# Performance work log

Measured on AMD Instinct MI355X. Metric: run time of the kernel, lower is better.

Reference implementation:

```python
import jax, jax.numpy as jnp
import numpy as np

N_NODES = 100000
N_EDGES = 3200000
N_FEAT = 512
HIDDEN = 16
N_CLASSES = 8


def setup_inputs() -> dict:
    key = jax.random.key(0)
    ks = jax.random.split(key, 7)
    x = jax.random.normal(ks[0], (N_NODES, N_FEAT), dtype=jnp.float32)
    edge_index = jax.random.randint(ks[1], (2, N_EDGES), 0, N_NODES, dtype=jnp.int64)
    # original code scales weights by /100; uniform weights are equivalent for testing
    edges_weight = jax.random.uniform(ks[2], (N_EDGES,), dtype=jnp.float32)
    # Glorot-ish params for the two GCNConv layers
    W1 = jax.random.normal(ks[3], (N_FEAT, HIDDEN), dtype=jnp.float32) / np.sqrt(N_FEAT)
    b1 = jnp.zeros((HIDDEN,), dtype=jnp.float32)
    W2 = jax.random.normal(ks[4], (HIDDEN, N_CLASSES), dtype=jnp.float32) / np.sqrt(HIDDEN)
    b2 = jnp.zeros((N_CLASSES,), dtype=jnp.float32)
    return {"x": x, "edge_index": edge_index, "edges_weight": edges_weight,
            "W1": W1, "b1": b1, "W2": W2, "b2": b2}


def _gcn_norm(edge_index, edges_weight, num_nodes):
    """PyG GCNConv normalization: add self-loops (weight 1), then
    norm_e = d^{-1/2}[src] * w_e * d^{-1/2}[dst] with d = weighted degree."""
    loop = jnp.arange(num_nodes, dtype=edge_index.dtype)
    src = jnp.concatenate([edge_index[0], loop])
    dst = jnp.concatenate([edge_index[1], loop])
    w = jnp.concatenate([edges_weight, jnp.ones((num_nodes,), edges_weight.dtype)])
    deg = jax.ops.segment_sum(w, dst, num_segments=num_nodes)
    dis = jnp.where(deg > 0, jax.lax.rsqrt(deg), 0.0)  # deg_inv_sqrt
    norm = dis[src] * w * dis[dst]
    return src, dst, norm


def _gcn_layer(h, W, b, src, dst, norm, num_nodes):
    h = h @ W                                 # transform first (small msg dim)
    msg = h[src] * norm[:, None]              # gather + edge scaling
    out = jax.ops.segment_sum(msg, dst, num_segments=num_nodes)  # scatter-add
    return out + b


def reference(x, edge_index, edges_weight, W1, b1, W2, b2):
    n = x.shape[0]
    src, dst, norm = _gcn_norm(edge_index, edges_weight, n)
    h = _gcn_layer(x, W1, b1, src, dst, norm, n)
    h = jax.nn.relu(h)
    h = _gcn_layer(h, W2, b2, src, dst, norm, n)
    return jax.nn.log_softmax(h, axis=1)
```

## Files before the change

kernel.cpp:

```cpp
#include <hip/hip_runtime.h>

#define TPB 256
constexpr int HID = 16;
constexpr int NC  = 8;

__device__ __forceinline__ void atomAddF(float* p, float v) {
    unsafeAtomicAdd(p, v);
}

__global__ void detect64_kernel(const int* __restrict__ ei, int E, int* flag) {
    int l = threadIdx.x;
    int v = 0;
    if (l < 32 && 2 * l + 1 < 2 * E) v = ei[2 * l + 1];
    unsigned long long b = __ballot(v != 0);
    if (l == 0) *flag = (b == 0ULL) ? 1 : 0;
}

__device__ __forceinline__ int edge_at(const int* __restrict__ ei, int index, int is64) {
    return is64 ? ei[2 * index] : ei[index];
}


__global__ void init_deg_kernel(float* deg, int N) {
    int i = blockIdx.x * TPB + threadIdx.x;
    if (i < N) deg[i] = 1.0f;
}

__global__ void init_nd_kernel(float* deg, int* cnt, int N) {
    int i = blockIdx.x * TPB + threadIdx.x;
    if (i < N) { deg[i] = 1.0f; cnt[i] = 0; }
}

__global__ void init_cnt_kernel(int* cnt, int N) {
    int i = blockIdx.x * TPB + threadIdx.x;
    if (i < N) cnt[i] = 0;
}

__global__ void dis_kernel(float* deg, int N) {
    int i = blockIdx.x * TPB + threadIdx.x;
    if (i < N) deg[i] = rsqrtf(deg[i]);
}

__global__ void gemm1_kernel(const float* __restrict__ x, const float* __restrict__ W,
                             float* __restrict__ h, int N, int K) {
    int row = blockIdx.x * TPB + threadIdx.x;
    if (row >= N) return;
    const float* xr = x + (size_t)row * K;
    float acc[HID];
#pragma unroll
    for (int j = 0; j < HID; ++j) acc[j] = 0.f;
    for (int k = 0; k < K; k += 4) {
        float4 xv = *reinterpret_cast<const float4*>(xr + k);
        const float* Wk = W + (size_t)k * HID;
#pragma unroll
        for (int kk = 0; kk < 4; ++kk) {
            float xs = (&xv.x)[kk];
#pragma unroll
            for (int j = 0; j < HID; ++j)
                acc[j] = fmaf(xs, Wk[kk * HID + j], acc[j]);
        }
    }
    float* hr = h + (size_t)row * HID;
#pragma unroll
    for (int j = 0; j < HID; j += 4)
        *reinterpret_cast<float4*>(hr + j) = make_float4(acc[j], acc[j+1], acc[j+2], acc[j+3]);
}

__global__ void gemm1s_kernel(const float* __restrict__ x, const float* __restrict__ W,
                              const float* __restrict__ dis, float* __restrict__ h, int N, int K) {
    int row = blockIdx.x * TPB + threadIdx.x;
    if (row >= N) return;
    const float* xr = x + (size_t)row * K;
    float acc[HID];
#pragma unroll
    for (int j = 0; j < HID; ++j) acc[j] = 0.f;
    for (int k = 0; k < K; k += 4) {
        float4 xv = *reinterpret_cast<const float4*>(xr + k);
        const float* Wk = W + (size_t)k * HID;
#pragma unroll
        for (int kk = 0; kk < 4; ++kk) {
            float xs = (&xv.x)[kk];
#pragma unroll
            for (int j = 0; j < HID; ++j)
                acc[j] = fmaf(xs, Wk[kk * HID + j], acc[j]);
        }
    }
    float d = dis[row];
#pragma unroll
    for (int j = 0; j < HID; ++j) acc[j] *= d;
    float* hr = h + (size_t)row * HID;
#pragma unroll
    for (int j = 0; j < HID; j += 4)
        *reinterpret_cast<float4*>(hr + j) = make_float4(acc[j], acc[j+1], acc[j+2], acc[j+3]);
}

__global__ void gemm2_kernel(const float* __restrict__ agg1, const float* __restrict__ W2,
                             float* __restrict__ h2, int N) {
    int i = blockIdx.x * TPB + threadIdx.x;
    if (i >= N) return;
    const float* a = agg1 + (size_t)i * HID;
    float hv[HID];
#pragma unroll
    for (int k = 0; k < HID; k += 4) {
        float4 v = *reinterpret_cast<const float4*>(a + k);
        hv[k]     = fmaxf(v.x, 0.f);
        hv[k + 1] = fmaxf(v.y, 0.f);
        hv[k + 2] = fmaxf(v.z, 0.f);
        hv[k + 3] = fmaxf(v.w, 0.f);
    }
    float acc[NC];
#pragma unroll
    for (int c = 0; c < NC; ++c) acc[c] = 0.f;
#pragma unroll
    for (int k = 0; k < HID; ++k)
#pragma unroll
        for (int c = 0; c < NC; ++c)
            acc[c] = fmaf(hv[k], W2[k * NC + c], acc[c]);
    float* o = h2 + (size_t)i * NC;
    *reinterpret_cast<float4*>(o)     = make_float4(acc[0], acc[1], acc[2], acc[3]);
    *reinterpret_cast<float4*>(o + 4) = make_float4(acc[4], acc[5], acc[6], acc[7]);
}

__global__ void gemm2s_kernel(const float* __restrict__ agg1, const float* __restrict__ W2,
                              const float* __restrict__ dis, float* __restrict__ h2, int N) {
    int i = blockIdx.x * TPB + threadIdx.x;
    if (i >= N) return;
    const float* a = agg1 + (size_t)i * HID;
    float hv[HID];
#pragma unroll
    for (int k = 0; k < HID; k += 4) {
        float4 v = *reinterpret_cast<const float4*>(a + k);
        hv[k]     = fmaxf(v.x, 0.f);
        hv[k + 1] = fmaxf(v.y, 0.f);
        hv[k + 2] = fmaxf(v.z, 0.f);
        hv[k + 3] = fmaxf(v.w, 0.f);
    }
    float acc[NC];
#pragma unroll
    for (int c = 0; c < NC; ++c) acc[c] = 0.f;
#pragma unroll
    for (int k = 0; k < HID; ++k)
#pragma unroll
        for (int c = 0; c < NC; ++c)
            acc[c] = fmaf(hv[k], W2[k * NC + c], acc[c]);
    float d = dis[i];
#pragma unroll
    for (int c = 0; c < NC; ++c) acc[c] *= d;
    float* o = h2 + (size_t)i * NC;
    *reinterpret_cast<float4*>(o)     = make_float4(acc[0], acc[1], acc[2], acc[3]);
    *reinterpret_cast<float4*>(o + 4) = make_float4(acc[4], acc[5], acc[6], acc[7]);
}


__global__ void scatterP_kernel(const int* __restrict__ ei, const float* __restrict__ w,
                                int* __restrict__ cnt, uint2* __restrict__ edata,
                                int E, int C, const int* __restrict__ flag) {
    int e = blockIdx.x * TPB + threadIdx.x;
    if (e >= E) return;
    int is64 = *flag;
    int src = edge_at(ei, e, is64);
    int dst = edge_at(ei, E + e, is64);
    float wv = w[e];
    int pos = atomicAdd(&cnt[dst], 1);
    if (pos < C)
        edata[(size_t)dst * C + pos] = make_uint2((unsigned)src, __float_as_uint(wv));
}

__global__ void degP_kernel(const uint2* __restrict__ edata, const int* __restrict__ cnt,
                            float* __restrict__ dis, int N, int C) {
    int wid = (blockIdx.x * blockDim.x + threadIdx.x) >> 6;
    if (wid >= N) return;
    int lane = threadIdx.x & 63;
    int m = cnt[wid]; if (m > C) m = C;
    const uint2* seg = edata + (size_t)wid * C;
    float s = 0.f;
    for (int i = lane; i < m; i += 64) s += __uint_as_float(seg[i].y);
#pragma unroll
    for (int o = 1; o < 64; o <<= 1) s += __shfl_xor(s, o, 64);
    if (lane == 0) dis[wid] = rsqrtf(1.0f + s);
}

__global__ void agg1P_kernel(const uint2* __restrict__ edata, const int* __restrict__ cnt,
                             const float* __restrict__ h1s, const float* __restrict__ dis,
                             const float* __restrict__ b1, float* __restrict__ agg1,
                             int N, int C) {
    int wid = (blockIdx.x * blockDim.x + threadIdx.x) >> 6;
    if (wid >= N) return;
    int lane = threadIdx.x & 63;
    int m = cnt[wid]; if (m > C) m = C;
    const uint2* seg = edata + (size_t)wid * C;
    float acc[HID];
#pragma unroll
    for (int j = 0; j < HID; ++j) acc[j] = 0.f;
    for (int i = lane; i < m; i += 64) {
        uint2 u = seg[i];
        float wv = __uint_as_float(u.y);
        const float* hr = h1s + (size_t)u.x * HID;
        float4 a = *reinterpret_cast<const float4*>(hr);
        float4 b = *reinterpret_cast<const float4*>(hr + 4);
        float4 c = *reinterpret_cast<const float4*>(hr + 8);
        float4 d = *reinterpret_cast<const float4*>(hr + 12);
        acc[0]  = fmaf(wv, a.x, acc[0]);  acc[1]  = fmaf(wv, a.y, acc[1]);
        acc[2]  = fmaf(wv, a.z, acc[2]);  acc[3]  = fmaf(wv, a.w, acc[3]);
        acc[4]  = fmaf(wv, b.x, acc[4]);  acc[5]  = fmaf(wv, b.y, acc[5]);
        acc[6]  = fmaf(wv, b.z, acc[6]);  acc[7]  = fmaf(wv, b.w, acc[7]);
        acc[8]  = fmaf(wv, c.x, acc[8]);  acc[9]  = fmaf(wv, c.y, acc[9]);
        acc[10] = fmaf(wv, c.z, acc[10]); acc[11] = fmaf(wv, c.w, acc[11]);
        acc[12] = fmaf(wv, d.x, acc[12]); acc[13] = fmaf(wv, d.y, acc[13]);
        acc[14] = fmaf(wv, d.z, acc[14]); acc[15] = fmaf(wv, d.w, acc[15]);
    }
#pragma unroll
    for (int j = 0; j < HID; ++j) {
        acc[j] += __shfl_xor(acc[j], 16, 64);
        acc[j] += __shfl_xor(acc[j], 32, 64);
    }
#pragma unroll
    for (int t = 0; t < 8; ++t) {
        float lo = __shfl_xor(acc[t], 8, 64);
        float hi = __shfl_xor(acc[t + 8], 8, 64);
        acc[t] = (lane & 8) ? (acc[t + 8] + hi) : (acc[t] + lo);
    }
#pragma unroll
    for (int t = 0; t < 4; ++t) {
        float lo = __shfl_xor(acc[t], 4, 64);
        float hi = __shfl_xor(acc[t + 4], 4, 64);
        acc[t] = (lane & 4) ? (acc[t + 4] + hi) : (acc[t] + lo);
    }
#pragma unroll
    for (int t = 0; t < 2; ++t) {
        float lo = __shfl_xor(acc[t], 2, 64);
        float hi = __shfl_xor(acc[t + 2], 2, 64);
        acc[t] = (lane & 2) ? (acc[t + 2] + hi) : (acc[t] + lo);
    }
    {
        float lo = __shfl_xor(acc[0], 1, 64);
        float hi = __shfl_xor(acc[1], 1, 64);
        acc[0] = (lane & 1) ? (acc[1] + hi) : (acc[0] + lo);
    }
    if (lane < HID) {
        float dd = dis[wid];
        agg1[(size_t)wid * HID + lane] =
            b1[lane] + dd * (h1s[(size_t)wid * HID + lane] + acc[0]);
    }
}

__global__ void agg2P_lsm_kernel(const uint2* __restrict__ edata, const int* __restrict__ cnt,
                                 const float* __restrict__ h2s, const float* __restrict__ dis,
                                 const float* __restrict__ b2, float* __restrict__ out,
                                 int N, int C) {
    int wid = (blockIdx.x * blockDim.x + threadIdx.x) >> 6;
    if (wid >= N) return;
    int lane = threadIdx.x & 63;
    int m = cnt[wid]; if (m > C) m = C;
    const uint2* seg = edata + (size_t)wid * C;
    float acc[NC];
#pragma unroll
    for (int j = 0; j < NC; ++j) acc[j] = 0.f;
    for (int i = lane; i < m; i += 64) {
        uint2 u = seg[i];
        float wv = __uint_as_float(u.y);
        const float* hr = h2s + (size_t)u.x * NC;
        float4 a = *reinterpret_cast<const float4*>(hr);
        float4 b = *reinterpret_cast<const float4*>(hr + 4);
        acc[0] = fmaf(wv, a.x, acc[0]);  acc[1] = fmaf(wv, a.y, acc[1]);
        acc[2] = fmaf(wv, a.z, acc[2]);  acc[3] = fmaf(wv, a.w, acc[3]);
        acc[4] = fmaf(wv, b.x, acc[4]);  acc[5] = fmaf(wv, b.y, acc[5]);
        acc[6] = fmaf(wv, b.z, acc[6]);  acc[7] = fmaf(wv, b.w, acc[7]);
    }
#pragma unroll
    for (int j = 0; j < NC; ++j) {
        acc[j] += __shfl_xor(acc[j], 8, 64);
        acc[j] += __shfl_xor(acc[j], 16, 64);
        acc[j] += __shfl_xor(acc[j], 32, 64);
    }
#pragma unroll
    for (int t = 0; t < 4; ++t) {
        float lo = __shfl_xor(acc[t], 4, 64);
        float hi = __shfl_xor(acc[t + 4], 4, 64);
        acc[t] = (lane & 4) ? (acc[t + 4] + hi) : (acc[t] + lo);
    }
#pragma unroll
    for (int t = 0; t < 2; ++t) {
        float lo = __shfl_xor(acc[t], 2, 64);
        float hi = __shfl_xor(acc[t + 2], 2, 64);
        acc[t] = (lane & 2) ? (acc[t + 2] + hi) : (acc[t] + lo);
    }
    {
        float lo = __shfl_xor(acc[0], 1, 64);
        float hi = __shfl_xor(acc[1], 1, 64);
        acc[0] = (lane & 1) ? (acc[1] + hi) : (acc[0] + lo);
    }
    int c = lane & 7;
    float dd = dis[wid];
    float v = b2[c] + dd * (h2s[(size_t)wid * NC + c] + acc[0]);
    float mx = v;
    mx = fmaxf(mx, __shfl_xor(mx, 1, 64));
    mx = fmaxf(mx, __shfl_xor(mx, 2, 64));
    mx = fmaxf(mx, __shfl_xor(mx, 4, 64));
    float ex = expf(v - mx);
    float ssum = ex;
    ssum += __shfl_xor(ssum, 1, 64);
    ssum += __shfl_xor(ssum, 2, 64);
    ssum += __shfl_xor(ssum, 4, 64);
    float r = v - mx - logf(ssum);
    if (lane < NC) out[(size_t)wid * NC + lane] = r;
}


__global__ void hist_deg_kernel(const int* __restrict__ ei, const float* __restrict__ w,
                                int* __restrict__ cnt, float* __restrict__ deg,
                                int E, const int* __restrict__ flag) {
    int e = blockIdx.x * TPB + threadIdx.x;
    if (e >= E) return;
    int is64 = *flag;
    int dst = edge_at(ei, E + e, is64);
    atomicAdd(&cnt[dst], 1);
    atomAddF(&deg[dst], w[e]);
}

__global__ void scanA_kernel(const int* __restrict__ cnt, int* __restrict__ bsum, int N) {
    int i = blockIdx.x * 256 + threadIdx.x;
    int v = (i < N) ? cnt[i] : 0;
#pragma unroll
    for (int o = 32; o > 0; o >>= 1) v += __shfl_down(v, o, 64);
    __shared__ int ws[4];
    if ((threadIdx.x & 63) == 0) ws[threadIdx.x >> 6] = v;
    __syncthreads();
    if (threadIdx.x == 0) bsum[blockIdx.x] = ws[0] + ws[1] + ws[2] + ws[3];
}

__global__ void scanB_kernel(int* __restrict__ bsum, int NB, int* __restrict__ rowoffN, int E) {
    __shared__ int s[1024];
    int t = threadIdx.x;
    int v = (t < NB) ? bsum[t] : 0;
    s[t] = v;
    __syncthreads();
    for (int o = 1; o < 1024; o <<= 1) {
        int u = (t >= o) ? s[t - o] : 0;
        __syncthreads();
        s[t] += u;
        __syncthreads();
    }
    if (t < NB) bsum[t] = s[t] - v;
    if (t == 0) *rowoffN = E;
}

__global__ void scanC_kernel(const int* __restrict__ cnt, const int* __restrict__ bsum,
                             int* __restrict__ rowoff, int* __restrict__ cursor, int N) {
    __shared__ int s[256];
    int b = blockIdx.x, t = threadIdx.x;
    int i = b * 256 + t;
    int v = (i < N) ? cnt[i] : 0;
    s[t] = v;
    __syncthreads();
    for (int o = 1; o < 256; o <<= 1) {
        int u = (t >= o) ? s[t - o] : 0;
        __syncthreads();
        s[t] += u;
        __syncthreads();
    }
    if (i < N) {
        int ex = bsum[b] + s[t] - v;
        rowoff[i] = ex;
        cursor[i] = ex;
    }
}

__global__ void scatter_kernel(const int* __restrict__ ei, const float* __restrict__ w,
                               const float* __restrict__ dis, int* __restrict__ cursor,
                               int2* __restrict__ edata, int E, const int* __restrict__ flag) {
    int e = blockIdx.x * TPB + threadIdx.x;
    if (e >= E) return;
    int is64 = *flag;
    int src = edge_at(ei, e, is64);
    int dst = edge_at(ei, E + e, is64);
    float nrm = dis[src] * w[e] * dis[dst];
    int pos = atomicAdd(&cursor[dst], 1);
    edata[pos] = make_int2(src, __float_as_int(nrm));
}

__global__ void agg1_csr_kernel(const int2* __restrict__ edata, const int* __restrict__ rowoff,
                                const float* __restrict__ h1, const float* __restrict__ dis,
                                const float* __restrict__ b1, float* __restrict__ agg1, int N) {
    int wid = (blockIdx.x * blockDim.x + threadIdx.x) >> 6;
    if (wid >= N) return;
    int lane = threadIdx.x & 63;
    int j = lane & 15, g = lane >> 4;
    int s = rowoff[wid];
    int epd = rowoff[wid + 1] - s;
    float acc = 0.f;
    for (int i = g; i < epd; i += 4) {
        int2 d = edata[s + i];
        acc += __int_as_float(d.y) * h1[(size_t)d.x * HID + j];
    }
    acc += __shfl_xor(acc, 16, 64);
    acc += __shfl_xor(acc, 32, 64);
    if (g == 0) {
        float di = dis[wid];
        agg1[(size_t)wid * HID + j] = b1[j] + di * di * h1[(size_t)wid * HID + j] + acc;
    }
}

__global__ void agg2_lsm_kernel(const int2* __restrict__ edata, const int* __restrict__ rowoff,
                                const float* __restrict__ h2, const float* __restrict__ dis,
                                const float* __restrict__ b2, float* __restrict__ out, int N) {
    int wid = (blockIdx.x * blockDim.x + threadIdx.x) >> 6;
    if (wid >= N) return;
    int lane = threadIdx.x & 63;
    int j = lane & 7, g = lane >> 3;
    int s = rowoff[wid];
    int epd = rowoff[wid + 1] - s;
    float acc = 0.f;
    for (int i = g; i < epd; i += 8) {
        int2 d = edata[s + i];
        acc += __int_as_float(d.y) * h2[(size_t)d.x * NC + j];
    }
    acc += __shfl_xor(acc, 8, 64);
    acc += __shfl_xor(acc, 16, 64);
    acc += __shfl_xor(acc, 32, 64);
    float di = dis[wid];
    float v = b2[j] + di * di * h2[(size_t)wid * NC + j] + acc;
    float mx = v;
    mx = fmaxf(mx, __shfl_xor(mx, 1, 64));
    mx = fmaxf(mx, __shfl_xor(mx, 2, 64));
    mx = fmaxf(mx, __shfl_xor(mx, 4, 64));
    float ex = expf(v - mx);
    float ssum = ex;
    ssum += __shfl_xor(ssum, 1, 64);
    ssum += __shfl_xor(ssum, 2, 64);
    ssum += __shfl_xor(ssum, 4, 64);
    float r = v - mx - logf(ssum);
    if (g == 0) out[(size_t)wid * NC + j] = r;
}


__global__ void deg_edge_kernel(const int* __restrict__ ei, const float* __restrict__ w,
                                float* deg, int E, const int* __restrict__ flag) {
    int e = blockIdx.x * TPB + threadIdx.x;
    if (e >= E) return;
    int is64 = *flag;
    int dst = edge_at(ei, E + e, is64);
    atomAddF(&deg[dst], w[e]);
}

__global__ void init_agg1_kernel(const float* __restrict__ h1, const float* __restrict__ dis,
                                 const float* __restrict__ b1, float* __restrict__ agg1, int N) {
    int t = blockIdx.x * TPB + threadIdx.x;
    if (t >= N * HID) return;
    int i = t >> 4, j = t & 15;
    float d = dis[i];
    agg1[t] = b1[j] + d * d * h1[t];
}

__global__ void edge1_kernel(const int* __restrict__ ei, const float* __restrict__ w,
                             const float* __restrict__ dis, const float* __restrict__ h1,
                             float* __restrict__ agg1, int E, const int* __restrict__ flag) {
    int t = blockIdx.x * TPB + threadIdx.x;
    if (t >= E * HID) return;
    int e = t >> 4, j = t & 15;
    int is64 = *flag;
    int src = edge_at(ei, e, is64);
    int dst = edge_at(ei, E + e, is64);
    float nrm = dis[src] * w[e] * dis[dst];
    atomAddF(&agg1[dst * HID + j], nrm * h1[src * HID + j]);
}

__global__ void init_out_kernel(const float* __restrict__ h2, const float* __restrict__ dis,
                                const float* __restrict__ b2, float* __restrict__ out, int N) {
    int t = blockIdx.x * TPB + threadIdx.x;
    if (t >= N * NC) return;
    int i = t >> 3, j = t & 7;
    float d = dis[i];
    out[t] = b2[j] + d * d * h2[t];
}

__global__ void edge2_kernel(const int* __restrict__ ei, const float* __restrict__ w,
                             const float* __restrict__ dis, const float* __restrict__ h2,
                             float* __restrict__ out, int E, const int* __restrict__ flag) {
    int t = blockIdx.x * TPB + threadIdx.x;
    if (t >= E * NC) return;
    int e = t >> 3, j = t & 7;
    int is64 = *flag;
    int src = edge_at(ei, e, is64);
    int dst = edge_at(ei, E + e, is64);
    float nrm = dis[src] * w[e] * dis[dst];
    atomAddF(&out[dst * NC + j], nrm * h2[src * NC + j]);
}

__global__ void lsm_kernel(float* __restrict__ out, int N) {
    int i = blockIdx.x * TPB + threadIdx.x;
    if (i >= N) return;
    float* r = out + (size_t)i * NC;
    float4 a = *reinterpret_cast<const float4*>(r);
    float4 b = *reinterpret_cast<const float4*>(r + 4);
    float v[NC] = {a.x, a.y, a.z, a.w, b.x, b.y, b.z, b.w};
    float m = v[0];
#pragma unroll
    for (int j = 1; j < NC; ++j) m = fmaxf(m, v[j]);
    float s = 0.f;
#pragma unroll
    for (int j = 0; j < NC; ++j) s += expf(v[j] - m);
    float lse = m + logf(s);
#pragma unroll
    for (int j = 0; j < NC; ++j) v[j] -= lse;
    *reinterpret_cast<float4*>(r)     = make_float4(v[0], v[1], v[2], v[3]);
    *reinterpret_cast<float4*>(r + 4) = make_float4(v[4], v[5], v[6], v[7]);
}

extern "C" void kernel_launch(void* const* d_in, const int* in_sizes, int n_in,
                              void* d_out, int out_size, void* d_ws, size_t ws_size,
                              hipStream_t stream) {
    const float* x  = (const float*)d_in[0];
    const int*   ei = (const int*)d_in[1];
    const float* w  = (const float*)d_in[2];
    const float* W1 = (const float*)d_in[3];
    const float* b1 = (const float*)d_in[4];
    const float* W2 = (const float*)d_in[5];
    const float* b2 = (const float*)d_in[6];
    float* out = (float*)d_out;

    int E = in_sizes[2];
    int N = out_size / NC;
    int K = in_sizes[0] / N;

    auto nb = [](long long n) { return (int)((n + TPB - 1) / TPB); };
    int waveblocks = (int)(((long long)N * 64 + TPB - 1) / TPB);

    int C = 0;
    {
        int cands[3] = {96, 88, 80};
        for (int ci = 0; ci < 3; ++ci) {
            size_t need = (size_t)4 * ((size_t)2 * N * cands[ci] + (size_t)42 * N + 1);
            if (ws_size >= need) { C = cands[ci]; break; }
        }
    }

    if (C > 0) {
        uint2* edata = (uint2*)d_ws;
        float* h1s   = (float*)(edata + (size_t)N * C);
        float* agg1  = h1s + (size_t)N * HID;
        float* h2s   = agg1 + (size_t)N * HID;
        float* dis   = h2s + (size_t)N * NC;
        int*   cnt   = (int*)(dis + N);
        int*   flag  = cnt + N;

        detect64_kernel<<<1, 64, 0, stream>>>(ei, E, flag);
        init_cnt_kernel<<<nb(N), TPB, 0, stream>>>(cnt, N);
        scatterP_kernel<<<nb(E), TPB, 0, stream>>>(ei, w, cnt, edata, E, C, flag);
        degP_kernel<<<waveblocks, TPB, 0, stream>>>(edata, cnt, dis, N, C);
        gemm1s_kernel<<<nb(N), TPB, 0, stream>>>(x, W1, dis, h1s, N, K);
        agg1P_kernel<<<waveblocks, TPB, 0, stream>>>(edata, cnt, h1s, dis, b1, agg1, N, C);
        gemm2s_kernel<<<nb(N), TPB, 0, stream>>>(agg1, W2, dis, h2s, N);
        agg2P_lsm_kernel<<<waveblocks, TPB, 0, stream>>>(edata, cnt, h2s, dis, b2, out, N, C);
        return;
    }

    int NB = (N + 255) / 256;
    size_t need_csr = (size_t)4 * ((size_t)2 * E + (size_t)43 * N + 1026);
    bool use_csr = (ws_size >= need_csr) && (NB <= 1024);

    if (use_csr) {
        int2*  edata  = (int2*)d_ws;
        float* deg    = (float*)(edata + E);
        float* h1     = deg + N;
        float* agg1   = h1 + (size_t)N * HID;
        float* h2     = agg1 + (size_t)N * HID;
        int*   cnt    = (int*)(h2 + (size_t)N * NC);
        int*   rowoff = cnt + N;
        int*   cursor = rowoff + N + 1;
        int*   bsum   = cursor + N;
        int*   flag   = bsum + 1024;

        detect64_kernel<<<1, 64, 0, stream>>>(ei, E, flag);
        init_nd_kernel<<<nb(N), TPB, 0, stream>>>(deg, cnt, N);
        hist_deg_kernel<<<nb(E), TPB, 0, stream>>>(ei, w, cnt, deg, E, flag);
        dis_kernel<<<nb(N), TPB, 0, stream>>>(deg, N);
        scanA_kernel<<<NB, 256, 0, stream>>>(cnt, bsum, N);
        scanB_kernel<<<1, 1024, 0, stream>>>(bsum, NB, rowoff + N, E);
        scanC_kernel<<<NB, 256, 0, stream>>>(cnt, bsum, rowoff, cursor, N);
        gemm1_kernel<<<nb(N), TPB, 0, stream>>>(x, W1, h1, N, K);
        scatter_kernel<<<nb(E), TPB, 0, stream>>>(ei, w, deg, cursor, edata, E, flag);
        agg1_csr_kernel<<<waveblocks, TPB, 0, stream>>>(edata, rowoff, h1, deg, b1, agg1, N);
        gemm2_kernel<<<nb(N), TPB, 0, stream>>>(agg1, W2, h2, N);
        agg2_lsm_kernel<<<waveblocks, TPB, 0, stream>>>(edata, rowoff, h2, deg, b2, out, N);
    } else {
        float* deg  = (float*)d_ws;
        float* h1   = deg + N;
        float* agg1 = h1 + (size_t)N * HID;
        float* h2   = agg1 + (size_t)N * HID;
        int*   flag = (int*)(h2 + (size_t)N * NC);

        detect64_kernel<<<1, 64, 0, stream>>>(ei, E, flag);
        init_deg_kernel<<<nb(N), TPB, 0, stream>>>(deg, N);
        deg_edge_kernel<<<nb(E), TPB, 0, stream>>>(ei, w, deg, E, flag);
        dis_kernel<<<nb(N), TPB, 0, stream>>>(deg, N);
        gemm1_kernel<<<nb(N), TPB, 0, stream>>>(x, W1, h1, N, K);
        init_agg1_kernel<<<nb((long long)N * HID), TPB, 0, stream>>>(h1, deg, b1, agg1, N);
        edge1_kernel<<<nb((long long)E * HID), TPB, 0, stream>>>(ei, w, deg, h1, agg1, E, flag);
        gemm2_kernel<<<nb(N), TPB, 0, stream>>>(agg1, W2, h2, N);
        init_out_kernel<<<nb((long long)N * NC), TPB, 0, stream>>>(h2, deg, b2, out, N);
        edge2_kernel<<<nb((long long)E * NC), TPB, 0, stream>>>(ei, w, deg, h2, out, E, flag);
        lsm_kernel<<<nb(N), TPB, 0, stream>>>(out, N);
    }
}
```

Measured before the change: 722.4 us.

## Compute first-layer GEMM with one wavefront per row and W in LDS

```diff
diff --git a/kernel.cpp b/kernel.cpp
--- a/kernel.cpp
+++ b/kernel.cpp
@@ -3,6 +3,7 @@
 #define TPB 256
 constexpr int HID = 16;
 constexpr int NC  = 8;
+constexpr int WPAD = 20;
 
 __device__ __forceinline__ void atomAddF(float* p, float v) {
     unsafeAtomicAdd(p, v);
@@ -92,6 +93,72 @@
 #pragma unroll
     for (int j = 0; j < HID; j += 4)
         *reinterpret_cast<float4*>(hr + j) = make_float4(acc[j], acc[j+1], acc[j+2], acc[j+3]);
+}
+
+__global__ void gemm1w_kernel(const float* __restrict__ x, const float* __restrict__ W,
+                              const float* __restrict__ dis, float* __restrict__ h,
+                              int N, int K, int nwaves) {
+    extern __shared__ float Wlds[];
+    int t = threadIdx.x;
+    for (int i = t; i < K * HID; i += TPB) {
+        int k = i >> 4, j = i & 15;
+        Wlds[k * WPAD + j] = W[i];
+    }
+    __syncthreads();
+    int lane = t & 63;
+    int gwave = (int)((blockIdx.x * (unsigned)TPB + t) >> 6);
+    for (int row = gwave; row < N; row += nwaves) {
+        const float* xr = x + (size_t)row * K;
+        float acc[HID];
+#pragma unroll
+        for (int j = 0; j < HID; ++j) acc[j] = 0.f;
+        for (int k0 = lane; k0 < K; k0 += 64) {
+            float xs = xr[k0];
+            const float* Wr = Wlds + k0 * WPAD;
+            float4 a = *reinterpret_cast<const float4*>(Wr);
+            float4 b = *reinterpret_cast<const float4*>(Wr + 4);
+            float4 c = *reinterpret_cast<const float4*>(Wr + 8);
+            float4 d = *reinterpret_cast<const float4*>(Wr + 12);
+            acc[0]  = fmaf(xs, a.x, acc[0]);  acc[1]  = fmaf(xs, a.y, acc[1]);
+            acc[2]  = fmaf(xs, a.z, acc[2]);  acc[3]  = fmaf(xs, a.w, acc[3]);
+            acc[4]  = fmaf(xs, b.x, acc[4]);  acc[5]  = fmaf(xs, b.y, acc[5]);
+            acc[6]  = fmaf(xs, b.z, acc[6]);  acc[7]  = fmaf(xs, b.w, acc[7]);
+            acc[8]  = fmaf(xs, c.x, acc[8]);  acc[9]  = fmaf(xs, c.y, acc[9]);
+            acc[10] = fmaf(xs, c.z, acc[10]); acc[11] = fmaf(xs, c.w, acc[11]);
+            acc[12] = fmaf(xs, d.x, acc[12]); acc[13] = fmaf(xs, d.y, acc[13]);
+            acc[14] = fmaf(xs, d.z, acc[14]); acc[15] = fmaf(xs, d.w, acc[15]);
+        }
+#pragma unroll
+        for (int j = 0; j < HID; ++j) {
+            acc[j] += __shfl_xor(acc[j], 16, 64);
+            acc[j] += __shfl_xor(acc[j], 32, 64);
+        }
+#pragma unroll
+        for (int tt = 0; tt < 8; ++tt) {
+            float lo = __shfl_xor(acc[tt], 8, 64);
+            float hi = __shfl_xor(acc[tt + 8], 8, 64);
+            acc[tt] = (lane & 8) ? (acc[tt + 8] + hi) : (acc[tt] + lo);
+        }
+#pragma unroll
+        for (int tt = 0; tt < 4; ++tt) {
+            float lo = __shfl_xor(acc[tt], 4, 64);
+            float hi = __shfl_xor(acc[tt + 4], 4, 64);
+            acc[tt] = (lane & 4) ? (acc[tt + 4] + hi) : (acc[tt] + lo);
+        }
+#pragma unroll
+        for (int tt = 0; tt < 2; ++tt) {
+            float lo = __shfl_xor(acc[tt], 2, 64);
+            float hi = __shfl_xor(acc[tt + 2], 2, 64);
+            acc[tt] = (lane & 2) ? (acc[tt + 2] + hi) : (acc[tt] + lo);
+        }
+        {
+            float lo = __shfl_xor(acc[0], 1, 64);
+            float hi = __shfl_xor(acc[1], 1, 64);
+            acc[0] = (lane & 1) ? (acc[1] + hi) : (acc[0] + lo);
+        }
+        if (lane < HID)
+            h[(size_t)row * HID + lane] = dis[row] * acc[0];
+    }
 }
 
 __global__ void gemm2_kernel(const float* __restrict__ agg1, const float* __restrict__ W2,
@@ -548,7 +615,16 @@
         init_cnt_kernel<<<nb(N), TPB, 0, stream>>>(cnt, N);
         scatterP_kernel<<<nb(E), TPB, 0, stream>>>(ei, w, cnt, edata, E, C, flag);
         degP_kernel<<<waveblocks, TPB, 0, stream>>>(edata, cnt, dis, N, C);
-        gemm1s_kernel<<<nb(N), TPB, 0, stream>>>(x, W1, dis, h1s, N, K);
+
+        size_t wlds_bytes = (size_t)K * WPAD * 4;
+        if ((K % 64) == 0 && wlds_bytes <= 64 * 1024) {
+            int g1blocks = 2048;
+            int nwaves = g1blocks * (TPB / 64);
+            gemm1w_kernel<<<g1blocks, TPB, wlds_bytes, stream>>>(x, W1, dis, h1s, N, K, nwaves);
+        } else {
+            gemm1s_kernel<<<nb(N), TPB, 0, stream>>>(x, W1, dis, h1s, N, K);
+        }
+
         agg1P_kernel<<<waveblocks, TPB, 0, stream>>>(edata, cnt, h1s, dis, b1, agg1, N, C);
         gemm2s_kernel<<<nb(N), TPB, 0, stream>>>(agg1, W2, dis, h2s, N);
         agg2P_lsm_kernel<<<waveblocks, TPB, 0, stream>>>(edata, cnt, h2s, dis, b2, out, N, C);
```

Measured after the change: 776.1 us. 1.07x slower.

## Replace per-node padded edge lists with block-partitioned edges and shared-memory aggregation

Applied to the files above, without the earlier changes.

```diff
diff --git a/kernel.cpp b/kernel.cpp
--- a/kernel.cpp
+++ b/kernel.cpp
@@ -3,6 +3,10 @@
 #define TPB 256
 constexpr int HID = 16;
 constexpr int NC  = 8;
+constexpr int NPB = 512;
+constexpr int LOG_NPB = 9;
+constexpr int MAXBK = 1024;
+constexpr int P1B = 512;
 
 __device__ __forceinline__ void atomAddF(float* p, float v) {
     unsafeAtomicAdd(p, v);
@@ -26,11 +30,6 @@
     if (i < N) deg[i] = 1.0f;
 }
 
-__global__ void init_nd_kernel(float* deg, int* cnt, int N) {
-    int i = blockIdx.x * TPB + threadIdx.x;
-    if (i < N) { deg[i] = 1.0f; cnt[i] = 0; }
-}
-
 __global__ void init_cnt_kernel(int* cnt, int N) {
     int i = blockIdx.x * TPB + threadIdx.x;
     if (i < N) cnt[i] = 0;
@@ -40,6 +39,7 @@
     int i = blockIdx.x * TPB + threadIdx.x;
     if (i < N) deg[i] = rsqrtf(deg[i]);
 }
+
 
 __global__ void gemm1_kernel(const float* __restrict__ x, const float* __restrict__ W,
                              float* __restrict__ h, int N, int K) {
@@ -149,6 +149,168 @@
     float* o = h2 + (size_t)i * NC;
     *reinterpret_cast<float4*>(o)     = make_float4(acc[0], acc[1], acc[2], acc[3]);
     *reinterpret_cast<float4*>(o + 4) = make_float4(acc[4], acc[5], acc[6], acc[7]);
+}
+
+
+__global__ void zero_tot_kernel(int* tot, int NBK) {
+    int i = blockIdx.x * TPB + threadIdx.x;
+    if (i < NBK) tot[i] = 0;
+}
+
+__global__ void p1hist_kernel(const int* __restrict__ ei, int* __restrict__ hist,
+                              int* __restrict__ tot, int E, int NBK,
+                              const int* __restrict__ flag) {
+    __shared__ int lh[MAXBK];
+    int t = threadIdx.x;
+    for (int i = t; i < NBK; i += TPB) lh[i] = 0;
+    __syncthreads();
+    int is64 = *flag;
+    int CH = (E + gridDim.x - 1) / gridDim.x;
+    int s = blockIdx.x * CH;
+    int e2 = min(E, s + CH);
+    for (int i = s + t; i < e2; i += TPB) {
+        int dst = edge_at(ei, E + i, is64);
+        atomicAdd(&lh[dst >> LOG_NPB], 1);
+    }
+    __syncthreads();
+    for (int i = t; i < NBK; i += TPB) {
+        int v = lh[i];
+        hist[(size_t)blockIdx.x * NBK + i] = v;
+        if (v) atomicAdd(&tot[i], v);
+    }
+}
+
+__global__ void p1scan_kernel(const int* __restrict__ tot, int* __restrict__ base,
+                              int* __restrict__ cursor, int NBK, int E) {
+    __shared__ int s[1024];
+    int t = threadIdx.x;
+    int v = (t < NBK) ? tot[t] : 0;
+    s[t] = v;
+    __syncthreads();
+    for (int o = 1; o < 1024; o <<= 1) {
+        int u = (t >= o) ? s[t - o] : 0;
+        __syncthreads();
+        s[t] += u;
+        __syncthreads();
+    }
+    if (t < NBK) { base[t] = s[t] - v; cursor[t] = s[t] - v; }
+    if (t == 0) base[NBK] = E;
+}
+
+__global__ void p1scatter_kernel(const int* __restrict__ ei, const float* __restrict__ w,
+                                 const int* __restrict__ hist, int* __restrict__ cursor,
+                                 uint2* __restrict__ part, int E, int NBK,
+                                 const int* __restrict__ flag) {
+    __shared__ int startk[MAXBK];
+    __shared__ int loc[MAXBK];
+    int t = threadIdx.x;
+    for (int i = t; i < NBK; i += TPB) {
+        int hv = hist[(size_t)blockIdx.x * NBK + i];
+        startk[i] = hv ? atomicAdd(&cursor[i], hv) : 0;
+        loc[i] = 0;
+    }
+    __syncthreads();
+    int is64 = *flag;
+    int CH = (E + gridDim.x - 1) / gridDim.x;
+    int s = blockIdx.x * CH;
+    int e2 = min(E, s + CH);
+    for (int i = s + t; i < e2; i += TPB) {
+        int src = edge_at(ei, i, is64);
+        int dst = edge_at(ei, E + i, is64);
+        float wv = w[i];
+        int k = dst >> LOG_NPB;
+        int dl = dst & (NPB - 1);
+        int pos = startk[k] + atomicAdd(&loc[k], 1);
+        part[pos] = make_uint2(__float_as_uint(wv), (unsigned)src | ((unsigned)dl << 17));
+    }
+}
+
+__global__ void degB_kernel(const uint2* __restrict__ part, const int* __restrict__ base,
+                            float* __restrict__ dis, int N) {
+    __shared__ float dacc[NPB];
+    int k = blockIdx.x, t = threadIdx.x;
+    for (int r = t; r < NPB; r += TPB) dacc[r] = 1.0f;
+    __syncthreads();
+    int s = base[k], e2 = base[k + 1];
+    for (int i = s + t; i < e2; i += TPB) {
+        uint2 en = part[i];
+        atomicAdd(&dacc[(en.y >> 17) & (NPB - 1)], __uint_as_float(en.x));
+    }
+    __syncthreads();
+    for (int r = t; r < NPB; r += TPB) {
+        int node = (k << LOG_NPB) + r;
+        if (node < N) dis[node] = rsqrtf(dacc[r]);
+    }
+}
+
+__global__ void aggB1_kernel(const uint2* __restrict__ part, const int* __restrict__ base,
+                             const float* __restrict__ h1s, const float* __restrict__ dis,
+                             const float* __restrict__ b1, float* __restrict__ agg1, int N) {
+    __shared__ float acc[NPB * 17];
+    int k = blockIdx.x, t = threadIdx.x;
+    for (int idx = t; idx < NPB * HID; idx += TPB) {
+        int r = idx >> 4, j = idx & 15;
+        int node = (k << LOG_NPB) + r;
+        acc[r * 17 + j] = (node < N) ? h1s[(size_t)node * HID + j] : 0.f;
+    }
+    __syncthreads();
+    int s = base[k], e2 = base[k + 1];
+    int g = t >> 4, j = t & 15;
+    for (int i = s + g; i < e2; i += 16) {
+        uint2 en = part[i];
+        float wv = __uint_as_float(en.x);
+        int src = en.y & 0x1FFFF;
+        int dl = (en.y >> 17) & (NPB - 1);
+        atomicAdd(&acc[dl * 17 + j], wv * h1s[(size_t)src * HID + j]);
+    }
+    __syncthreads();
+    for (int idx = t; idx < NPB * HID; idx += TPB) {
+        int r = idx >> 4, jj = idx & 15;
+        int node = (k << LOG_NPB) + r;
+        if (node < N)
+            agg1[(size_t)node * HID + jj] = b1[jj] + dis[node] * acc[r * 17 + jj];
+    }
+}
+
+__global__ void aggB2_lsm_kernel(const uint2* __restrict__ part, const int* __restrict__ base,
+                                 const float* __restrict__ h2s, const float* __restrict__ dis,
+                                 const float* __restrict__ b2, float* __restrict__ out, int N) {
+    __shared__ float acc[NPB * 9];
+    int k = blockIdx.x, t = threadIdx.x;
+    for (int idx = t; idx < NPB * NC; idx += TPB) {
+        int r = idx >> 3, j = idx & 7;
+        int node = (k << LOG_NPB) + r;
+        acc[r * 9 + j] = (node < N) ? h2s[(size_t)node * NC + j] : 0.f;
+    }
+    __syncthreads();
+    int s = base[k], e2 = base[k + 1];
+    int g = t >> 3, j = t & 7;
+    for (int i = s + g; i < e2; i += 32) {
+        uint2 en = part[i];
+        float wv = __uint_as_float(en.x);
+        int src = en.y & 0x1FFFF;
+        int dl = (en.y >> 17) & (NPB - 1);
+        atomicAdd(&acc[dl * 9 + j], wv * h2s[(size_t)src * NC + j]);
+    }
+    __syncthreads();
+    for (int r = t; r < NPB; r += TPB) {
+        int node = (k << LOG_NPB) + r;
+        if (node >= N) continue;
+        float dd = dis[node];
+        float v[NC];
+#pragma unroll
+        for (int c = 0; c < NC; ++c) v[c] = b2[c] + dd * acc[r * 9 + c];
+        float m = v[0];
+#pragma unroll
+        for (int c = 1; c < NC; ++c) m = fmaxf(m, v[c]);
+        float ssum = 0.f;
+#pragma unroll
+        for (int c = 0; c < NC; ++c) ssum += expf(v[c] - m);
+        float lse = m + logf(ssum);
+        float* o = out + (size_t)node * NC;
+        *reinterpret_cast<float4*>(o)     = make_float4(v[0]-lse, v[1]-lse, v[2]-lse, v[3]-lse);
+        *reinterpret_cast<float4*>(o + 4) = make_float4(v[4]-lse, v[5]-lse, v[6]-lse, v[7]-lse);
+    }
 }
 
 
@@ -307,133 +469,6 @@
 }
 
 
-__global__ void hist_deg_kernel(const int* __restrict__ ei, const float* __restrict__ w,
-                                int* __restrict__ cnt, float* __restrict__ deg,
-                                int E, const int* __restrict__ flag) {
-    int e = blockIdx.x * TPB + threadIdx.x;
-    if (e >= E) return;
-    int is64 = *flag;
-    int dst = edge_at(ei, E + e, is64);
-    atomicAdd(&cnt[dst], 1);
-    atomAddF(&deg[dst], w[e]);
-}
-
-__global__ void scanA_kernel(const int* __restrict__ cnt, int* __restrict__ bsum, int N) {
-    int i = blockIdx.x * 256 + threadIdx.x;
-    int v = (i < N) ? cnt[i] : 0;
-#pragma unroll
-    for (int o = 32; o > 0; o >>= 1) v += __shfl_down(v, o, 64);
-    __shared__ int ws[4];
-    if ((threadIdx.x & 63) == 0) ws[threadIdx.x >> 6] = v;
-    __syncthreads();
-    if (threadIdx.x == 0) bsum[blockIdx.x] = ws[0] + ws[1] + ws[2] + ws[3];
-}
-
-__global__ void scanB_kernel(int* __restrict__ bsum, int NB, int* __restrict__ rowoffN, int E) {
-    __shared__ int s[1024];
-    int t = threadIdx.x;
-    int v = (t < NB) ? bsum[t] : 0;
-    s[t] = v;
-    __syncthreads();
-    for (int o = 1; o < 1024; o <<= 1) {
-        int u = (t >= o) ? s[t - o] : 0;
-        __syncthreads();
-        s[t] += u;
-        __syncthreads();
-    }
-    if (t < NB) bsum[t] = s[t] - v;
-    if (t == 0) *rowoffN = E;
-}
-
-__global__ void scanC_kernel(const int* __restrict__ cnt, const int* __restrict__ bsum,
-                             int* __restrict__ rowoff, int* __restrict__ cursor, int N) {
-    __shared__ int s[256];
-    int b = blockIdx.x, t = threadIdx.x;
-    int i = b * 256 + t;
-    int v = (i < N) ? cnt[i] : 0;
-    s[t] = v;
-    __syncthreads();
-    for (int o = 1; o < 256; o <<= 1) {
-        int u = (t >= o) ? s[t - o] : 0;
-        __syncthreads();
-        s[t] += u;
-        __syncthreads();
-    }
-    if (i < N) {
-        int ex = bsum[b] + s[t] - v;
-        rowoff[i] = ex;
-        cursor[i] = ex;
-    }
-}
-
-__global__ void scatter_kernel(const int* __restrict__ ei, const float* __restrict__ w,
-                               const float* __restrict__ dis, int* __restrict__ cursor,
-                               int2* __restrict__ edata, int E, const int* __restrict__ flag) {
-    int e = blockIdx.x * TPB + threadIdx.x;
-    if (e >= E) return;
-    int is64 = *flag;
-    int src = edge_at(ei, e, is64);
-    int dst = edge_at(ei, E + e, is64);
-    float nrm = dis[src] * w[e] * dis[dst];
-    int pos = atomicAdd(&cursor[dst], 1);
-    edata[pos] = make_int2(src, __float_as_int(nrm));
-}
-
-__global__ void agg1_csr_kernel(const int2* __restrict__ edata, const int* __restrict__ rowoff,
-                                const float* __restrict__ h1, const float* __restrict__ dis,
-                                const float* __restrict__ b1, float* __restrict__ agg1, int N) {
-    int wid = (blockIdx.x * blockDim.x + threadIdx.x) >> 6;
-    if (wid >= N) return;
-    int lane = threadIdx.x & 63;
-    int j = lane & 15, g = lane >> 4;
-    int s = rowoff[wid];
-    int epd = rowoff[wid + 1] - s;
-    float acc = 0.f;
-    for (int i = g; i < epd; i += 4) {
-        int2 d = edata[s + i];
-        acc += __int_as_float(d.y) * h1[(size_t)d.x * HID + j];
-    }
-    acc += __shfl_xor(acc, 16, 64);
-    acc += __shfl_xor(acc, 32, 64);
-    if (g == 0) {
-        float di = dis[wid];
-        agg1[(size_t)wid * HID + j] = b1[j] + di * di * h1[(size_t)wid * HID + j] + acc;
-    }
-}
-
-__global__ void agg2_lsm_kernel(const int2* __restrict__ edata, const int* __restrict__ rowoff,
-                                const float* __restrict__ h2, const float* __restrict__ dis,
-                                const float* __restrict__ b2, float* __restrict__ out, int N) {
-    int wid = (blockIdx.x * blockDim.x + threadIdx.x) >> 6;
-    if (wid >= N) return;
-    int lane = threadIdx.x & 63;
-    int j = lane & 7, g = lane >> 3;
-    int s = rowoff[wid];
-    int epd = rowoff[wid + 1] - s;
-    float acc = 0.f;
-    for (int i = g; i < epd; i += 8) {
-        int2 d = edata[s + i];
-        acc += __int_as_float(d.y) * h2[(size_t)d.x * NC + j];
-    }
-    acc += __shfl_xor(acc, 8, 64);
-    acc += __shfl_xor(acc, 16, 64);
-    acc += __shfl_xor(acc, 32, 64);
-    float di = dis[wid];
-    float v = b2[j] + di * di * h2[(size_t)wid * NC + j] + acc;
-    float mx = v;
-    mx = fmaxf(mx, __shfl_xor(mx, 1, 64));
-    mx = fmaxf(mx, __shfl_xor(mx, 2, 64));
-    mx = fmaxf(mx, __shfl_xor(mx, 4, 64));
-    float ex = expf(v - mx);
-    float ssum = ex;
-    ssum += __shfl_xor(ssum, 1, 64);
-    ssum += __shfl_xor(ssum, 2, 64);
-    ssum += __shfl_xor(ssum, 4, 64);
-    float r = v - mx - logf(ssum);
-    if (g == 0) out[(size_t)wid * NC + j] = r;
-}
-
-
 __global__ void deg_edge_kernel(const int* __restrict__ ei, const float* __restrict__ w,
                                 float* deg, int E, const int* __restrict__ flag) {
     int e = blockIdx.x * TPB + threadIdx.x;
@@ -524,7 +559,36 @@
     int K = in_sizes[0] / N;
 
     auto nb = [](long long n) { return (int)((n + TPB - 1) / TPB); };
-    int waveblocks = (int)(((long long)N * 64 + TPB - 1) / TPB);
+
+    int NBK = (N + NPB - 1) >> LOG_NPB;
+    size_t need_part = (size_t)4 * ((size_t)2 * E + (size_t)41 * N
+                                    + (size_t)P1B * NBK + 3 * (size_t)NBK + 8);
+    bool okpart = (N <= (1 << 17)) && (NBK <= MAXBK) && (ws_size >= need_part);
+
+    if (okpart) {
+        uint2* part  = (uint2*)d_ws;
+        float* h1s   = (float*)(part + E);
+        float* agg1  = h1s + (size_t)N * HID;
+        float* h2s   = agg1 + (size_t)N * HID;
+        float* dis   = h2s + (size_t)N * NC;
+        int*   hist  = (int*)(dis + N);
+        int*   tot   = hist + (size_t)P1B * NBK;
+        int*   base  = tot + NBK;
+        int*   cursor= base + NBK + 1;
+        int*   flag  = cursor + NBK;
+
+        detect64_kernel<<<1, 64, 0, stream>>>(ei, E, flag);
+        zero_tot_kernel<<<nb(NBK), TPB, 0, stream>>>(tot, NBK);
+        p1hist_kernel<<<P1B, TPB, 0, stream>>>(ei, hist, tot, E, NBK, flag);
+        p1scan_kernel<<<1, 1024, 0, stream>>>(tot, base, cursor, NBK, E);
+        p1scatter_kernel<<<P1B, TPB, 0, stream>>>(ei, w, hist, cursor, part, E, NBK, flag);
+        degB_kernel<<<NBK, TPB, 0, stream>>>(part, base, dis, N);
+        gemm1s_kernel<<<nb(N), TPB, 0, stream>>>(x, W1, dis, h1s, N, K);
+        aggB1_kernel<<<NBK, TPB, 0, stream>>>(part, base, h1s, dis, b1, agg1, N);
+        gemm2s_kernel<<<nb(N), TPB, 0, stream>>>(agg1, W2, dis, h2s, N);
+        aggB2_lsm_kernel<<<NBK, TPB, 0, stream>>>(part, base, h2s, dis, b2, out, N);
+        return;
+    }
 
     int C = 0;
     {
@@ -534,6 +598,7 @@
             if (ws_size >= need) { C = cands[ci]; break; }
         }
     }
+    int waveblocks = (int)(((long long)N * 64 + TPB - 1) / TPB);
 
     if (C > 0) {
         uint2* edata = (uint2*)d_ws;
@@ -555,35 +620,7 @@
         return;
     }
 
-    int NB = (N + 255) / 256;
-    size_t need_csr = (size_t)4 * ((size_t)2 * E + (size_t)43 * N + 1026);
-    bool use_csr = (ws_size >= need_csr) && (NB <= 1024);
-
-    if (use_csr) {
-        int2*  edata  = (int2*)d_ws;
-        float* deg    = (float*)(edata + E);
-        float* h1     = deg + N;
-        float* agg1   = h1 + (size_t)N * HID;
-        float* h2     = agg1 + (size_t)N * HID;
-        int*   cnt    = (int*)(h2 + (size_t)N * NC);
-        int*   rowoff = cnt + N;
-        int*   cursor = rowoff + N + 1;
-        int*   bsum   = cursor + N;
-        int*   flag   = bsum + 1024;
-
-        detect64_kernel<<<1, 64, 0, stream>>>(ei, E, flag);
-        init_nd_kernel<<<nb(N), TPB, 0, stream>>>(deg, cnt, N);
-        hist_deg_kernel<<<nb(E), TPB, 0, stream>>>(ei, w, cnt, deg, E, flag);
-        dis_kernel<<<nb(N), TPB, 0, stream>>>(deg, N);
-        scanA_kernel<<<NB, 256, 0, stream>>>(cnt, bsum, N);
-        scanB_kernel<<<1, 1024, 0, stream>>>(bsum, NB, rowoff + N, E);
-        scanC_kernel<<<NB, 256, 0, stream>>>(cnt, bsum, rowoff, cursor, N);
-        gemm1_kernel<<<nb(N), TPB, 0, stream>>>(x, W1, h1, N, K);
-        scatter_kernel<<<nb(E), TPB, 0, stream>>>(ei, w, deg, cursor, edata, E, flag);
-        agg1_csr_kernel<<<waveblocks, TPB, 0, stream>>>(edata, rowoff, h1, deg, b1, agg1, N);
-        gemm2_kernel<<<nb(N), TPB, 0, stream>>>(agg1, W2, h2, N);
-        agg2_lsm_kernel<<<waveblocks, TPB, 0, stream>>>(edata, rowoff, h2, deg, b2, out, N);
-    } else {
+    {
         float* deg  = (float*)d_ws;
         float* h1   = deg + N;
         float* agg1 = h1 + (size_t)N * HID;
```

Result: slower. 1.199 ms (+65.9%).
